# Kernel tuning notes

Measured on AMD Instinct MI355X. Metric: run time of the kernel, lower is better.

Reference implementation:

```python
import jax, jax.numpy as jnp
import numpy as np

NUM_STEPS = 128
STEP = 1.0 / (NUM_STEPS - 1)
N, D = 262144, 128


def setup_inputs() -> dict:
    key = jax.random.key(0)
    k0, k1, k2 = jax.random.split(key, 3)
    return {
        "feat_t0": jax.random.normal(k0, (N, D), dtype=jnp.float32),
        "feat_t1": jax.random.normal(k1, (N, D), dtype=jnp.float32),
        "label": jax.random.randint(k2, (N,), 0, 2),
    }


def _histogram(s, idx, inds, size):
    # s: [N] similarities in [0,1]; idx: [N] = floor(s/step) bin index (constant wrt grad)
    # t_j = j*STEP, j in [0, NUM_STEPS). Matches the torch masked-assign logic:
    #   indsa: delta == t - step  ->  w = (s - t + step)/step
    #   indsb: delta == t         ->  w = (-s + t + step)/step
    #   else 0; masked by class indicator `inds`; sum over samples / size.
    j = jnp.arange(NUM_STEPS, dtype=jnp.int32)[:, None]      # [T,1]
    t = j.astype(s.dtype) * STEP                              # [T,1]
    indsa = (idx[None, :] == (j - 1)) & inds[None, :]         # [T,N]
    indsb = (idx[None, :] == j) & inds[None, :]               # [T,N]
    wa = (s[None, :] - t + STEP) / STEP                       # [T,N]
    wb = (-s[None, :] + t + STEP) / STEP                      # [T,N]
    w = jnp.where(indsa, wa, 0.0) + jnp.where(indsb, wb, 0.0)
    return w.sum(axis=1) / size                               # [T]


def reference(feat_t0, feat_t1, label):
    # cosine similarity between the two temporal feature maps, mapped to [0,1]
    n0 = feat_t0 / jnp.linalg.norm(feat_t0, axis=1, keepdims=True)
    n1 = feat_t1 / jnp.linalg.norm(feat_t1, axis=1, keepdims=True)
    sim = jnp.sum(n0 * n1, axis=1)                            # [N] in [-1,1]
    s = jnp.clip((sim + 1.0) * 0.5, 0.0, 1.0)                 # [N] in [0,1]
    idx = jnp.floor(s / STEP).astype(jnp.int32)               # bin index (delta = idx*step)

    pos = label == 1  # changed pixels
    neg = label == 0  # unchanged pixels
    pos_size = jnp.maximum(pos.sum(), 1).astype(s.dtype)
    neg_size = jnp.maximum(neg.sum(), 1).astype(s.dtype)

    hist_pos = _histogram(s, idx, pos, pos_size)              # [T]
    hist_neg = _histogram(s, idx, neg, neg_size)              # [T]

    # histogram loss: probability that a negative similarity exceeds a positive one
    loss = jnp.sum(jnp.cumsum(hist_pos) * hist_neg)
    return loss
```

## Files before the change

kernel.cpp:

```cpp
#include <hip/hip_runtime.h>
#include <stdint.h>

#define T 128
#define STEPF (1.0f/127.0f)
#define NCOPY 8
#define WSSTRIDE 258


#define GLOAD(gp, lp) __builtin_amdgcn_global_load_lds(                        \
    (const __attribute__((address_space(1))) void*)(gp),                       \
    (__attribute__((address_space(3))) void*)(lp), 16, 0, 0)

__global__ __launch_bounds__(256) void sim_hist_kernel(
    const float* __restrict__ A, const float* __restrict__ B,
    const int* __restrict__ label, float* __restrict__ ws, int n) {
  __shared__ __align__(16) float tile[16384];
  __shared__ float hloc[2 * T];
  __shared__ unsigned int ccnt;
  const int tid = threadIdx.x;
  hloc[tid] = 0.0f;
  if (tid == 0) ccnt = 0u;
  __syncthreads();

  const int w      = tid >> 6;
  const int lam    = tid & 63;
  const int lhalf  = lam >> 5;
  const int c32    = lam & 31;
  const int g      = tid >> 2;
  const int gl     = g & 15;
  const int l      = tid & 3;
  const size_t rowbase = (size_t)blockIdx.x * 64 + w * 16;

  const int lv = label[blockIdx.x * 64 + g];

#pragma unroll
  for (int i = 0; i < 8; ++i) {
    const int r  = 2 * i + lhalf;
    const int cg = c32 ^ ((r & 7) << 2);
    GLOAD(A + (rowbase + r) * 128 + cg * 4, &tile[w * 4096 + i * 256]);
  }
#pragma unroll
  for (int i = 0; i < 8; ++i) {
    const int r  = 2 * i + lhalf;
    const int cg = c32 ^ ((r & 7) << 2);
    GLOAD(B + (rowbase + r) * 128 + cg * 4, &tile[w * 4096 + 2048 + i * 256]);
  }
  asm volatile("s_waitcnt vmcnt(0)" ::: "memory");
  __builtin_amdgcn_sched_barrier(0);

  const float* At = &tile[w * 4096 + gl * 128];
  const float* Bt = &tile[w * 4096 + 2048 + gl * 128];
  const int sw = (gl & 7) << 2;
  float ab = 0.f, aa = 0.f, bb = 0.f;
#pragma unroll
  for (int k = 0; k < 8; ++k) {
    const int c = (l + 4 * k) ^ sw;
    const float4 va = *(const float4*)&At[c * 4];
    const float4 vb = *(const float4*)&Bt[c * 4];
    ab = fmaf(va.x, vb.x, fmaf(va.y, vb.y, fmaf(va.z, vb.z, fmaf(va.w, vb.w, ab))));
    aa = fmaf(va.x, va.x, fmaf(va.y, va.y, fmaf(va.z, va.z, fmaf(va.w, va.w, aa))));
    bb = fmaf(vb.x, vb.x, fmaf(vb.y, vb.y, fmaf(vb.z, vb.z, fmaf(vb.w, vb.w, bb))));
  }
  ab += __shfl_xor(ab, 1); ab += __shfl_xor(ab, 2);
  aa += __shfl_xor(aa, 1); aa += __shfl_xor(aa, 2);
  bb += __shfl_xor(bb, 1); bb += __shfl_xor(bb, 2);

  int cnt = 0;
  if (l == 0) {
    const int lab = (lv == 1) ? 1 : 0;
    cnt = lab;
    const float sim = ab * rsqrtf(aa * bb);
    float s = fminf(fmaxf((sim + 1.0f) * 0.5f, 0.0f), 1.0f);
    const float idxf = floorf(s / STEPF);
    const int idx = (int)idxf;
    const float w0 = (-s + idxf * STEPF + STEPF) / STEPF;
    atomicAdd(&hloc[lab * T + idx], w0);
    if (idx + 1 < T) {
      const float w1 = (s - (idxf + 1.0f) * STEPF + STEPF) / STEPF;
      atomicAdd(&hloc[lab * T + idx + 1], w1);
    }
  }

#pragma unroll
  for (int off = 32; off > 0; off >>= 1) cnt += __shfl_xor(cnt, off);
  if (lam == 0 && cnt) atomicAdd(&ccnt, (unsigned int)cnt);
  __syncthreads();

  float* wsc = ws + (blockIdx.x & (NCOPY - 1)) * WSSTRIDE;
  const float v = hloc[tid];
  if (v != 0.0f) atomicAdd(&wsc[tid], v);
  if (tid == 0 && ccnt) atomicAdd((unsigned int*)(wsc + 2 * T), ccnt);
}

__global__ void finalize_kernel(const float* __restrict__ ws, float* __restrict__ out, int n) {
  const int lane = threadIdx.x & 63;
  unsigned int cpos = 0;
  float hp0 = 0.f, hp1 = 0.f, hn0 = 0.f, hn1 = 0.f;
  const int j0 = 2 * lane, j1 = 2 * lane + 1;
#pragma unroll
  for (int c = 0; c < NCOPY; ++c) {
    const float* wsc = ws + c * WSSTRIDE;
    hn0 += wsc[j0];       hn1 += wsc[j1];
    hp0 += wsc[T + j0];   hp1 += wsc[T + j1];
    cpos += ((const unsigned int*)(wsc + 2 * T))[0];
  }
  const float possz = fmaxf((float)cpos, 1.0f);
  const float negsz = fmaxf((float)(n - (int)cpos), 1.0f);
  hp0 /= possz; hp1 /= possz;
  hn0 /= negsz; hn1 /= negsz;

  const float pair = hp0 + hp1;
  float scan = pair;
#pragma unroll
  for (int off = 1; off < 64; off <<= 1) {
    const float u = __shfl_up(scan, off);
    if (lane >= off) scan += u;
  }
  const float excl = scan - pair;
  float part = (excl + hp0) * hn0 + (excl + hp0 + hp1) * hn1;
#pragma unroll
  for (int off = 32; off > 0; off >>= 1) part += __shfl_xor(part, off);
  if (lane == 0) out[0] = part;
}

extern "C" void kernel_launch(void* const* d_in, const int* in_sizes, int n_in,
                              void* d_out, int out_size, void* d_ws, size_t ws_size,
                              hipStream_t stream) {
  const float* A  = (const float*)d_in[0];
  const float* B  = (const float*)d_in[1];
  const int* lab  = (const int*)d_in[2];
  const int n = in_sizes[2];
  float* ws = (float*)d_ws;

  hipMemsetAsync(d_ws, 0, NCOPY * WSSTRIDE * sizeof(float), stream);

  const int grid = n >> 6;
  sim_hist_kernel<<<grid, 256, 0, stream>>>(A, B, lab, ws, n);
  finalize_kernel<<<1, 64, 0, stream>>>(ws, (float*)d_out, n);
}
```

Before: 52.46 us.

## Fuse finalize into histogram kernel via last-block completion counter

```diff
diff --git a/kernel.cpp b/kernel.cpp
--- a/kernel.cpp
+++ b/kernel.cpp
@@ -3,7 +3,7 @@
 
 #define T 128
 #define STEPF (1.0f/127.0f)
-#define NCOPY 8
+#define NCOPY 16
 #define WSSTRIDE 258
 
 
@@ -11,12 +11,16 @@
     (const __attribute__((address_space(1))) void*)(gp),                       \
     (__attribute__((address_space(3))) void*)(lp), 16, 0, 0)
 
+#define AGLOADF(p) __hip_atomic_load((p), __ATOMIC_RELAXED, __HIP_MEMORY_SCOPE_AGENT)
+
 __global__ __launch_bounds__(256) void sim_hist_kernel(
     const float* __restrict__ A, const float* __restrict__ B,
-    const int* __restrict__ label, float* __restrict__ ws, int n) {
+    const int* __restrict__ label, float* __restrict__ ws,
+    float* __restrict__ out, int n, int nblocks) {
   __shared__ __align__(16) float tile[16384];
   __shared__ float hloc[2 * T];
   __shared__ unsigned int ccnt;
+  __shared__ bool amLast;
   const int tid = threadIdx.x;
   hloc[tid] = 0.0f;
   if (tid == 0) ccnt = 0u;
@@ -86,41 +90,52 @@
   if (lam == 0 && cnt) atomicAdd(&ccnt, (unsigned int)cnt);
   __syncthreads();
 
+  unsigned int* cntp  = (unsigned int*)(ws + NCOPY * WSSTRIDE);
+  unsigned int* donep = cntp + 1;
+
   float* wsc = ws + (blockIdx.x & (NCOPY - 1)) * WSSTRIDE;
   const float v = hloc[tid];
   if (v != 0.0f) atomicAdd(&wsc[tid], v);
-  if (tid == 0 && ccnt) atomicAdd((unsigned int*)(wsc + 2 * T), ccnt);
-}
+  if (tid == 0 && ccnt) atomicAdd(cntp, ccnt);
 
-__global__ void finalize_kernel(const float* __restrict__ ws, float* __restrict__ out, int n) {
-  const int lane = threadIdx.x & 63;
-  unsigned int cpos = 0;
-  float hp0 = 0.f, hp1 = 0.f, hn0 = 0.f, hn1 = 0.f;
-  const int j0 = 2 * lane, j1 = 2 * lane + 1;
+  asm volatile("s_waitcnt vmcnt(0)" ::: "memory");
+  __syncthreads();
+
+  if (tid == 0) {
+    const unsigned int prev = atomicAdd(donep, 1u);
+    amLast = (prev == (unsigned int)(nblocks - 1));
+  }
+  __syncthreads();
+
+  if (amLast && tid < 64) {
+    const int lane = tid;
+    const int j0 = 2 * lane, j1 = 2 * lane + 1;
+    float hp0 = 0.f, hp1 = 0.f, hn0 = 0.f, hn1 = 0.f;
 #pragma unroll
-  for (int c = 0; c < NCOPY; ++c) {
-    const float* wsc = ws + c * WSSTRIDE;
-    hn0 += wsc[j0];       hn1 += wsc[j1];
-    hp0 += wsc[T + j0];   hp1 += wsc[T + j1];
-    cpos += ((const unsigned int*)(wsc + 2 * T))[0];
+    for (int c = 0; c < NCOPY; ++c) {
+      const float* wc = ws + c * WSSTRIDE;
+      hn0 += AGLOADF(wc + j0);     hn1 += AGLOADF(wc + j1);
+      hp0 += AGLOADF(wc + T + j0); hp1 += AGLOADF(wc + T + j1);
+    }
+    const unsigned int cpos = __hip_atomic_load(cntp, __ATOMIC_RELAXED, __HIP_MEMORY_SCOPE_AGENT);
+    const float possz = fmaxf((float)cpos, 1.0f);
+    const float negsz = fmaxf((float)(n - (int)cpos), 1.0f);
+    hp0 /= possz; hp1 /= possz;
+    hn0 /= negsz; hn1 /= negsz;
+
+    const float pair = hp0 + hp1;
+    float scan = pair;
+#pragma unroll
+    for (int off = 1; off < 64; off <<= 1) {
+      const float u = __shfl_up(scan, off);
+      if (lane >= off) scan += u;
+    }
+    const float excl = scan - pair;
+    float part = (excl + hp0) * hn0 + (excl + hp0 + hp1) * hn1;
+#pragma unroll
+    for (int off = 32; off > 0; off >>= 1) part += __shfl_xor(part, off);
+    if (lane == 0) out[0] = part;
   }
-  const float possz = fmaxf((float)cpos, 1.0f);
-  const float negsz = fmaxf((float)(n - (int)cpos), 1.0f);
-  hp0 /= possz; hp1 /= possz;
-  hn0 /= negsz; hn1 /= negsz;
-
-  const float pair = hp0 + hp1;
-  float scan = pair;
-#pragma unroll
-  for (int off = 1; off < 64; off <<= 1) {
-    const float u = __shfl_up(scan, off);
-    if (lane >= off) scan += u;
-  }
-  const float excl = scan - pair;
-  float part = (excl + hp0) * hn0 + (excl + hp0 + hp1) * hn1;
-#pragma unroll
-  for (int off = 32; off > 0; off >>= 1) part += __shfl_xor(part, off);
-  if (lane == 0) out[0] = part;
 }
 
 extern "C" void kernel_launch(void* const* d_in, const int* in_sizes, int n_in,
@@ -132,9 +147,8 @@
   const int n = in_sizes[2];
   float* ws = (float*)d_ws;
 
-  hipMemsetAsync(d_ws, 0, NCOPY * WSSTRIDE * sizeof(float), stream);
+  hipMemsetAsync(d_ws, 0, (NCOPY * WSSTRIDE + 2) * sizeof(float), stream);
 
   const int grid = n >> 6;
-  sim_hist_kernel<<<grid, 256, 0, stream>>>(A, B, lab, ws, n);
-  finalize_kernel<<<1, 64, 0, stream>>>(ws, (float*)d_out, n);
+  sim_hist_kernel<<<grid, 256, 0, stream>>>(A, B, lab, ws, (float*)d_out, n, grid);
 }
```

New measurement: 118.8 us. +126.5%, slower.
